# Kernel tuning notes

Hardware: AMD Instinct MI355X
Metric: run time of the kernel (lower is better)

The kernel has to match this reference:

```python
import jax, jax.numpy as jnp
import numpy as np

TOPK_R = 32  # topk_R from init


def setup_inputs() -> dict:
    key = jax.random.key(0)
    k1, k2 = jax.random.split(key)
    B, N, L_in, L_out = 8, 2048, 512, 512
    x = jax.random.normal(k1, (B, N, L_in), dtype=jnp.float32)
    # kaiming-uniform-style init for Linear weight [out, in]
    bound = float(np.sqrt(6.0 / L_in))
    W = jax.random.uniform(k2, (L_out, L_in), dtype=jnp.float32, minval=-bound, maxval=bound)
    return {"x": x, "W": W}


def reference(x, W):
    # x: [B, N, L_in]; W: [L_out, L_in] (Linear, no bias)
    xp = jnp.einsum('bnl,ol->bno', x, W)          # [B, N, L_out]
    # sim_score with norm=False: plain dot product
    score = jnp.einsum('bnd,bmd->bnm', xp, xp)    # [B, N, N]
    B, N, _ = score.shape
    # RkNNAdjacency: identity + top-k neighbors per row set to 1
    topk_idx = jax.lax.top_k(score, TOPK_R)[1]    # [B, N, k]
    adj = jnp.broadcast_to(jnp.eye(N, dtype=score.dtype), (B, N, N))
    b_idx = jnp.arange(B)[:, None, None]
    n_idx = jnp.arange(N)[None, :, None]
    adj = adj.at[b_idx, n_idx, topk_idx].set(1.0)
    # mask: 1 where neighbor, -1e19 elsewhere; NOTE: multiplicative mask (mask * score)
    mask = jnp.where(adj == 1.0, jnp.ones_like(adj), jnp.full_like(adj, -1e19))
    attention = jax.nn.softmax(mask * score, axis=2)  # [B, N, N]
    h = jnp.einsum('bnm,bmd->bnd', attention, xp)     # [B, N, L_out]
    return (h, attention)
```

## Files before the change

### kernel.cpp

```cpp
#include <hip/hip_runtime.h>
#include <cfloat>


typedef short bf16x8 __attribute__((ext_vector_type(8)));
typedef _Float16 f16x8 __attribute__((ext_vector_type(8)));
typedef _Float16 f16x4 __attribute__((ext_vector_type(4)));
typedef float f32x4 __attribute__((ext_vector_type(4)));

#define NX4 2097152
#define NW4 65536

__device__ __forceinline__ unsigned short f2bf(float f) {
  unsigned int u = __float_as_uint(f);
  unsigned int r = (u + 0x7FFFu + ((u >> 16) & 1u)) >> 16;
  return (unsigned short)r;
}

__device__ __forceinline__ void gload_lds16(const unsigned short* g, unsigned short* l) {
  __builtin_amdgcn_global_load_lds(
      (const __attribute__((address_space(1))) unsigned int*)g,
      (__attribute__((address_space(3))) unsigned int*)l, 16, 0, 0);
}

__device__ __forceinline__ unsigned int skey(float v, int m) {
  unsigned int u = __float_as_uint(v);
  u ^= ((unsigned int)((int)u >> 31)) | 0x80000000u;
  return (u & 0xFFFFF800u) | (unsigned int)m;
}

__global__ __launch_bounds__(256) void split_kernel(const float* __restrict__ x,
                                                    const float* __restrict__ W,
                                                    _Float16* __restrict__ xh,
                                                    _Float16* __restrict__ xl,
                                                    _Float16* __restrict__ wh,
                                                    _Float16* __restrict__ wl) {
  const int idx = blockIdx.x * 256 + threadIdx.x;
  if (idx >= NX4 + NW4) return;
  const bool isx = idx < NX4;
  const int i4 = isx ? idx : idx - NX4;
  const float4 v = isx ? reinterpret_cast<const float4*>(x)[i4]
                       : reinterpret_cast<const float4*>(W)[i4];
  f16x4 hv, lv;
  const float vv[4] = {v.x, v.y, v.z, v.w};
#pragma unroll
  for (int c = 0; c < 4; ++c) {
    const _Float16 h = (_Float16)vv[c];
    hv[c] = h;
    lv[c] = (_Float16)((vv[c] - (float)h) * 2048.0f);
  }
  if (isx) {
    reinterpret_cast<f16x4*>(xh)[i4] = hv;
    reinterpret_cast<f16x4*>(xl)[i4] = lv;
  } else {
    reinterpret_cast<f16x4*>(wh)[i4] = hv;
    reinterpret_cast<f16x4*>(wl)[i4] = lv;
  }
}

__global__ __launch_bounds__(256, 2) void gemm_xw_mfma(const unsigned short* __restrict__ xh,
                                                       const unsigned short* __restrict__ xl,
                                                       const unsigned short* __restrict__ wh,
                                                       const unsigned short* __restrict__ wl,
                                                       float* __restrict__ xp,
                                                       unsigned short* __restrict__ xp16) {
  __shared__ unsigned short lAh[2][128 * 32];
  __shared__ unsigned short lAl[2][128 * 32];
  __shared__ unsigned short lBh[2][128 * 32];
  __shared__ unsigned short lBl[2][128 * 32];
  const int tid = threadIdx.x;
  const int wid = tid >> 6, lane = tid & 63;
  const int lr = lane & 15, kg = lane >> 4;
  const int nbase = blockIdx.x * 128;
  const int obase = blockIdx.y * 128;
  const int wr = wid >> 1, wc = wid & 1;

  const int srow = tid >> 2;
  const int scol = (tid & 3) * 8;
  const unsigned short* gAh0 = xh + (size_t)(nbase + srow) * 512 + scol;
  const unsigned short* gAh1 = xh + (size_t)(nbase + 64 + srow) * 512 + scol;
  const unsigned short* gAl0 = xl + (size_t)(nbase + srow) * 512 + scol;
  const unsigned short* gAl1 = xl + (size_t)(nbase + 64 + srow) * 512 + scol;
  const unsigned short* gBh0 = wh + (size_t)(obase + srow) * 512 + scol;
  const unsigned short* gBh1 = wh + (size_t)(obase + 64 + srow) * 512 + scol;
  const unsigned short* gBl0 = wl + (size_t)(obase + srow) * 512 + scol;
  const unsigned short* gBl1 = wl + (size_t)(obase + 64 + srow) * 512 + scol;

  f32x4 acc_hh[4][4] = {};
  f32x4 acc_x[4][4] = {};

#define K1_STAGE(KB, BUF)                                  \
  do {                                                     \
    gload_lds16(gAh0 + (KB), &lAh[BUF][wid * 512]);        \
    gload_lds16(gAh1 + (KB), &lAh[BUF][2048 + wid * 512]); \
    gload_lds16(gAl0 + (KB), &lAl[BUF][wid * 512]);        \
    gload_lds16(gAl1 + (KB), &lAl[BUF][2048 + wid * 512]); \
    gload_lds16(gBh0 + (KB), &lBh[BUF][wid * 512]);        \
    gload_lds16(gBh1 + (KB), &lBh[BUF][2048 + wid * 512]); \
    gload_lds16(gBl0 + (KB), &lBl[BUF][wid * 512]);        \
    gload_lds16(gBl1 + (KB), &lBl[BUF][2048 + wid * 512]); \
  } while (0)

#define K1_COMPUTE(BUF)                                                                \
  do {                                                                                 \
    f16x8 ah[4], al[4], bh[4], bl[4];                                                  \
    _Pragma("unroll") for (int i2 = 0; i2 < 4; ++i2) {                                 \
      ah[i2] = *reinterpret_cast<const f16x8*>(&lAh[BUF][(wr * 64 + i2 * 16 + lr) * 32 + kg * 8]); \
      al[i2] = *reinterpret_cast<const f16x8*>(&lAl[BUF][(wr * 64 + i2 * 16 + lr) * 32 + kg * 8]); \
      bh[i2] = *reinterpret_cast<const f16x8*>(&lBh[BUF][(wc * 64 + i2 * 16 + lr) * 32 + kg * 8]); \
      bl[i2] = *reinterpret_cast<const f16x8*>(&lBl[BUF][(wc * 64 + i2 * 16 + lr) * 32 + kg * 8]); \
    }                                                                                  \
    _Pragma("unroll") for (int i2 = 0; i2 < 4; ++i2)                                   \
        _Pragma("unroll") for (int j2 = 0; j2 < 4; ++j2) {                             \
      acc_hh[i2][j2] = __builtin_amdgcn_mfma_f32_16x16x32_f16(ah[i2], bh[j2], acc_hh[i2][j2], 0, 0, 0); \
      acc_x[i2][j2] = __builtin_amdgcn_mfma_f32_16x16x32_f16(ah[i2], bl[j2], acc_x[i2][j2], 0, 0, 0);   \
      acc_x[i2][j2] = __builtin_amdgcn_mfma_f32_16x16x32_f16(al[i2], bh[j2], acc_x[i2][j2], 0, 0, 0);   \
    }                                                                                  \
  } while (0)

  K1_STAGE(0, 0);
  __syncthreads();
  for (int t = 0; t < 15; ++t) {
    K1_STAGE((t + 1) * 32, (t & 1) ^ 1);
    K1_COMPUTE(t & 1);
    __syncthreads();
  }
  K1_COMPUTE(1);

#pragma unroll
  for (int i = 0; i < 4; ++i) {
#pragma unroll
    for (int j = 0; j < 4; ++j) {
#pragma unroll
      for (int r = 0; r < 4; ++r) {
        const float v = acc_hh[i][j][r] + acc_x[i][j][r] * (1.0f / 2048.0f);
        const size_t row = (size_t)(nbase + wr * 64 + i * 16 + kg * 4 + r);
        const int col = obase + wc * 64 + j * 16 + lr;
        xp[row * 512 + col] = v;
        xp16[row * 512 + col] = f2bf(v);
      }
    }
  }
#undef K1_STAGE
#undef K1_COMPUTE
}

__global__ __launch_bounds__(256) void score_kernel(const unsigned short* __restrict__ xp16,
                                                    unsigned int* __restrict__ cand) {
  __shared__ unsigned short lA[2][128 * 32];
  __shared__ unsigned short lB[2][128 * 32];
  const int tid = threadIdx.x;
  const int wid = tid >> 6, lane = tid & 63;
  const int lr = lane & 15, kg = lane >> 4;
  const int b = blockIdx.x & 7;
  int p = blockIdx.x >> 3;
  int tn = 0, rem = 16;
  while (p >= rem) { p -= rem; rem--; tn++; }
  const int tm = tn + p;
  const int nbase = tn * 128, mbase = tm * 128;
  const unsigned short* Xb = xp16 + (size_t)b * 2048 * 512;
  const int wr = wid >> 1, wc = wid & 1;

  const int srow = tid >> 2;
  const int scol = (tid & 3) * 8;
  const unsigned short* gA0 = Xb + (size_t)(nbase + srow) * 512 + scol;
  const unsigned short* gA1 = Xb + (size_t)(nbase + 64 + srow) * 512 + scol;
  const unsigned short* gB0 = Xb + (size_t)(mbase + srow) * 512 + scol;
  const unsigned short* gB1 = Xb + (size_t)(mbase + 64 + srow) * 512 + scol;

  f32x4 acc[4][4] = {};

#define STAGE(KB, BUF)                                    \
  do {                                                    \
    gload_lds16(gA0 + (KB), &lA[BUF][wid * 512]);         \
    gload_lds16(gA1 + (KB), &lA[BUF][2048 + wid * 512]);  \
    gload_lds16(gB0 + (KB), &lB[BUF][wid * 512]);         \
    gload_lds16(gB1 + (KB), &lB[BUF][2048 + wid * 512]);  \
  } while (0)

#define COMPUTE(BUF)                                                                   \
  do {                                                                                 \
    bf16x8 af[4], bfr[4];                                                              \
    _Pragma("unroll") for (int i2 = 0; i2 < 4; ++i2) {                                 \
      af[i2] = *reinterpret_cast<const bf16x8*>(&lA[BUF][(wr * 64 + i2 * 16 + lr) * 32 + kg * 8]); \
      bfr[i2] = *reinterpret_cast<const bf16x8*>(&lB[BUF][(wc * 64 + i2 * 16 + lr) * 32 + kg * 8]); \
    }                                                                                  \
    _Pragma("unroll") for (int i2 = 0; i2 < 4; ++i2)                                   \
        _Pragma("unroll") for (int j2 = 0; j2 < 4; ++j2)                               \
            acc[i2][j2] =                                                              \
                __builtin_amdgcn_mfma_f32_16x16x32_bf16(af[i2], bfr[j2], acc[i2][j2], 0, 0, 0); \
  } while (0)

  STAGE(0, 0);
  __syncthreads();
  for (int t = 0; t < 15; ++t) {
    STAGE((t + 1) * 32, (t & 1) ^ 1);
    COMPUTE(t & 1);
    __syncthreads();
  }
  COMPUTE(1);

  const int mcol = mbase + wc * 64 + lr;
#pragma unroll
  for (int i = 0; i < 4; ++i) {
#pragma unroll
    for (int r = 0; r < 4; ++r) {
      const unsigned int x0 = skey(acc[i][0][r], mcol + 0);
      const unsigned int x1 = skey(acc[i][1][r], mcol + 16);
      const unsigned int x2 = skey(acc[i][2][r], mcol + 32);
      const unsigned int x3 = skey(acc[i][3][r], mcol + 48);
      const unsigned int lo01 = min(x0, x1), hi01 = max(x0, x1);
      const unsigned int lo23 = min(x2, x3), hi23 = max(x2, x3);
      unsigned int k1 = min(lo01, lo23);
      unsigned int k2 = min(max(lo01, lo23), min(hi01, hi23));
#pragma unroll
      for (int off = 1; off < 16; off <<= 1) {
        const unsigned int o1 = (unsigned int)__shfl_xor((int)k1, off);
        const unsigned int o2 = (unsigned int)__shfl_xor((int)k2, off);
        const unsigned int nk1 = min(k1, o1);
        const unsigned int nk2 = min(max(k1, o1), min(k2, o2));
        k1 = nk1;
        k2 = nk2;
      }
      if (lr == 0) {
        const int n = nbase + wr * 64 + i * 16 + kg * 4 + r;
        const uint2 kv = {k1, k2};
        *reinterpret_cast<uint2*>(cand + ((size_t)b * 2048 + n) * 512 + (tm * 2 + wc) * 2) = kv;
      }
    }
  }

  if (tn != tm) {
    const int nrow0 = nbase + wr * 64 + kg * 4;
#pragma unroll
    for (int j = 0; j < 4; ++j) {
      unsigned int k1 = 0xFFFFFFFFu, k2 = 0xFFFFFFFFu;
#pragma unroll
      for (int i = 0; i < 4; ++i) {
#pragma unroll
        for (int r = 0; r < 4; ++r) {
          const unsigned int xk = skey(acc[i][j][r], nrow0 + i * 16 + r);
          const unsigned int nk1 = min(k1, xk);
          k2 = min(k2, max(k1, xk));
          k1 = nk1;
        }
      }
#pragma unroll
      for (int off = 16; off < 64; off <<= 1) {
        const unsigned int o1 = (unsigned int)__shfl_xor((int)k1, off);
        const unsigned int o2 = (unsigned int)__shfl_xor((int)k2, off);
        const unsigned int nk1 = min(k1, o1);
        const unsigned int nk2 = min(max(k1, o1), min(k2, o2));
        k1 = nk1;
        k2 = nk2;
      }
      if (kg == 0) {
        const int m = mbase + wc * 64 + j * 16 + lr;
        const uint2 kv = {k1, k2};
        *reinterpret_cast<uint2*>(cand + ((size_t)b * 2048 + m) * 512 + (tn * 2 + wr) * 2) = kv;
      }
    }
  }
#undef STAGE
#undef COMPUTE
}

__global__ __launch_bounds__(64) void finalize_kernel(const float* __restrict__ xp,
                                                      float* __restrict__ h,
                                                      float* __restrict__ att) {
  const int l = threadIdx.x;
  const int b = blockIdx.x & 7;
  const int n = blockIdx.x >> 3;
  const size_t r = (size_t)b * 2048 + n;

  unsigned int key = reinterpret_cast<const unsigned int*>(h + r * 512)[l];
  int wsel[8];
#pragma unroll
  for (int t = 0; t < 8; ++t) {
    unsigned int m = key;
#pragma unroll
    for (int off = 1; off < 64; off <<= 1)
      m = min(m, (unsigned int)__shfl_xor((int)m, off));
    wsel[t] = (int)(m & 0x7FFu);
    if (key == m) key = 0xFFFFFFFFu;
  }

  const float* xb = xp + (size_t)b * 2048 * 512;
  const float* xn = xb + (size_t)n * 512;
  const float4 q0 = reinterpret_cast<const float4*>(xn)[2 * l];
  const float4 q1 = reinterpret_cast<const float4*>(xn)[2 * l + 1];

  float bestv = FLT_MAX;
  int besti = 0x7fffffff;
#pragma unroll
  for (int t = 0; t < 8; ++t) {
    const float* xm = xb + (size_t)wsel[t] * 512;
    const float4 p0 = reinterpret_cast<const float4*>(xm)[2 * l];
    const float4 p1 = reinterpret_cast<const float4*>(xm)[2 * l + 1];
    float s = 0.f;
    s = fmaf(q0.x, p0.x, s); s = fmaf(q0.y, p0.y, s);
    s = fmaf(q0.z, p0.z, s); s = fmaf(q0.w, p0.w, s);
    s = fmaf(q1.x, p1.x, s); s = fmaf(q1.y, p1.y, s);
    s = fmaf(q1.z, p1.z, s); s = fmaf(q1.w, p1.w, s);
#pragma unroll
    for (int off = 1; off < 64; off <<= 1) s += __shfl_xor(s, off);
    if (s < bestv || (s == bestv && wsel[t] < besti)) { bestv = s; besti = wsel[t]; }
  }

  const float* xs = xb + (size_t)besti * 512;
  const float4 w0 = reinterpret_cast<const float4*>(xs)[2 * l];
  const float4 w1 = reinterpret_cast<const float4*>(xs)[2 * l + 1];
  float* hrow = h + r * 512;
  reinterpret_cast<float4*>(hrow)[2 * l] = w0;
  reinterpret_cast<float4*>(hrow)[2 * l + 1] = w1;

  float* arow = att + r * 2048;
#pragma unroll
  for (int s = 0; s < 8; ++s) {
    const int cbase = s * 256 + l * 4;
    float4 v;
    v.x = (cbase + 0 == besti) ? 1.0f : 0.0f;
    v.y = (cbase + 1 == besti) ? 1.0f : 0.0f;
    v.z = (cbase + 2 == besti) ? 1.0f : 0.0f;
    v.w = (cbase + 3 == besti) ? 1.0f : 0.0f;
    reinterpret_cast<float4*>(arow)[s * 64 + l] = v;
  }
}

extern "C" void kernel_launch(void* const* d_in, const int* in_sizes, int n_in,
                              void* d_out, int out_size, void* d_ws, size_t ws_size,
                              hipStream_t stream) {
  const float* x = (const float*)d_in[0];
  const float* W = (const float*)d_in[1];
  float* out = (float*)d_out;
  float* h = out;
  float* att = out + (size_t)8 * 2048 * 512;
  float* xp = (float*)d_ws;

  char* attb = (char*)att;
  _Float16* xh = (_Float16*)(attb + 0);
  _Float16* xl = (_Float16*)(attb + (size_t)16 * 1024 * 1024);
  _Float16* wh = (_Float16*)(attb + (size_t)32 * 1024 * 1024);
  _Float16* wl = (_Float16*)(attb + (size_t)33 * 1024 * 1024);
  unsigned short* xp16 = (unsigned short*)(attb + (size_t)112 * 1024 * 1024);

  hipLaunchKernelGGL(split_kernel, dim3((NX4 + NW4 + 255) / 256), dim3(256), 0, stream,
                     x, W, xh, xl, wh, wl);

  hipLaunchKernelGGL(gemm_xw_mfma, dim3(16384 / 128, 512 / 128), dim3(256), 0, stream,
                     (const unsigned short*)xh, (const unsigned short*)xl,
                     (const unsigned short*)wh, (const unsigned short*)wl, xp, xp16);

  hipLaunchKernelGGL(score_kernel, dim3(8 * 136), dim3(256), 0, stream, xp16,
                     (unsigned int*)h);

  hipLaunchKernelGGL(finalize_kernel, dim3(16384), dim3(64), 0, stream, xp, h, att);
}
```

Baseline: 124.6 us.

## Fuse x fp16 hi/lo split into the projection GEMM's A-tile load

The separate pass that splits all of x into fp16 high/low halves is removed. The GEMM now loads fp32 x tiles into registers, splits them in-kernel and writes them to LDS, overlapped with the MFMA compute on the other buffer. Only W is still pre-split. This avoids a 32MB read and 32MB write round trip through global memory. In exchange the GEMM reads fp32 A four times, once per output column block, and does extra conversion ALU work and register-staged LDS stores in its loop.

```diff
diff --git a/kernel.cpp b/kernel.cpp
--- a/kernel.cpp
+++ b/kernel.cpp
@@ -7,7 +7,6 @@
 typedef _Float16 f16x4 __attribute__((ext_vector_type(4)));
 typedef float f32x4 __attribute__((ext_vector_type(4)));
 
-#define NX4 2097152
 #define NW4 65536
 
 __device__ __forceinline__ unsigned short f2bf(float f) {
@@ -28,18 +27,12 @@
   return (u & 0xFFFFF800u) | (unsigned int)m;
 }
 
-__global__ __launch_bounds__(256) void split_kernel(const float* __restrict__ x,
-                                                    const float* __restrict__ W,
-                                                    _Float16* __restrict__ xh,
-                                                    _Float16* __restrict__ xl,
-                                                    _Float16* __restrict__ wh,
-                                                    _Float16* __restrict__ wl) {
-  const int idx = blockIdx.x * 256 + threadIdx.x;
-  if (idx >= NX4 + NW4) return;
-  const bool isx = idx < NX4;
-  const int i4 = isx ? idx : idx - NX4;
-  const float4 v = isx ? reinterpret_cast<const float4*>(x)[i4]
-                       : reinterpret_cast<const float4*>(W)[i4];
+__global__ __launch_bounds__(256) void splitW_kernel(const float* __restrict__ W,
+                                                     _Float16* __restrict__ wh,
+                                                     _Float16* __restrict__ wl) {
+  const int i4 = blockIdx.x * 256 + threadIdx.x;
+  if (i4 >= NW4) return;
+  const float4 v = reinterpret_cast<const float4*>(W)[i4];
   f16x4 hv, lv;
   const float vv[4] = {v.x, v.y, v.z, v.w};
 #pragma unroll
@@ -48,17 +41,11 @@
     hv[c] = h;
     lv[c] = (_Float16)((vv[c] - (float)h) * 2048.0f);
   }
-  if (isx) {
-    reinterpret_cast<f16x4*>(xh)[i4] = hv;
-    reinterpret_cast<f16x4*>(xl)[i4] = lv;
-  } else {
-    reinterpret_cast<f16x4*>(wh)[i4] = hv;
-    reinterpret_cast<f16x4*>(wl)[i4] = lv;
-  }
-}
-
-__global__ __launch_bounds__(256, 2) void gemm_xw_mfma(const unsigned short* __restrict__ xh,
-                                                       const unsigned short* __restrict__ xl,
+  reinterpret_cast<f16x4*>(wh)[i4] = hv;
+  reinterpret_cast<f16x4*>(wl)[i4] = lv;
+}
+
+__global__ __launch_bounds__(256, 2) void gemm_xw_mfma(const float* __restrict__ x,
                                                        const unsigned short* __restrict__ wh,
                                                        const unsigned short* __restrict__ wl,
                                                        float* __restrict__ xp,
@@ -76,10 +63,8 @@
 
   const int srow = tid >> 2;
   const int scol = (tid & 3) * 8;
-  const unsigned short* gAh0 = xh + (size_t)(nbase + srow) * 512 + scol;
-  const unsigned short* gAh1 = xh + (size_t)(nbase + 64 + srow) * 512 + scol;
-  const unsigned short* gAl0 = xl + (size_t)(nbase + srow) * 512 + scol;
-  const unsigned short* gAl1 = xl + (size_t)(nbase + 64 + srow) * 512 + scol;
+  const float* gX0 = x + (size_t)(nbase + srow) * 512 + scol;
+  const float* gX1 = x + (size_t)(nbase + 64 + srow) * 512 + scol;
   const unsigned short* gBh0 = wh + (size_t)(obase + srow) * 512 + scol;
   const unsigned short* gBh1 = wh + (size_t)(obase + 64 + srow) * 512 + scol;
   const unsigned short* gBl0 = wl + (size_t)(obase + srow) * 512 + scol;
@@ -87,13 +72,37 @@
 
   f32x4 acc_hh[4][4] = {};
   f32x4 acc_x[4][4] = {};
-
-#define K1_STAGE(KB, BUF)                                  \
+  float4 va[4];
+
+#define K1_LOADA(KB)                                                \
+  do {                                                              \
+    va[0] = *reinterpret_cast<const float4*>(gX0 + (KB));           \
+    va[1] = *reinterpret_cast<const float4*>(gX0 + (KB) + 4);       \
+    va[2] = *reinterpret_cast<const float4*>(gX1 + (KB));           \
+    va[3] = *reinterpret_cast<const float4*>(gX1 + (KB) + 4);       \
+  } while (0)
+
+#define K1_WRITEA(BUF)                                              \
+  do {                                                              \
+    _Pragma("unroll") for (int p = 0; p < 2; ++p) {                 \
+      f16x8 hv, lv;                                                 \
+      _Pragma("unroll") for (int q = 0; q < 2; ++q) {               \
+        const float vv[4] = {va[2 * p + q].x, va[2 * p + q].y,      \
+                             va[2 * p + q].z, va[2 * p + q].w};     \
+        _Pragma("unroll") for (int c = 0; c < 4; ++c) {             \
+          const _Float16 hh = (_Float16)vv[c];                      \
+          hv[4 * q + c] = hh;                                       \
+          lv[4 * q + c] = (_Float16)((vv[c] - (float)hh) * 2048.0f);\
+        }                                                           \
+      }                                                             \
+      const int ra = (srow + 64 * p) * 32 + scol;                   \
+      *reinterpret_cast<f16x8*>(&lAh[BUF][ra]) = hv;                \
+      *reinterpret_cast<f16x8*>(&lAl[BUF][ra]) = lv;                \
+    }                                                               \
+  } while (0)
+
+#define K1_STAGEB(KB, BUF)                                 \
   do {                                                     \
-    gload_lds16(gAh0 + (KB), &lAh[BUF][wid * 512]);        \
-    gload_lds16(gAh1 + (KB), &lAh[BUF][2048 + wid * 512]); \
-    gload_lds16(gAl0 + (KB), &lAl[BUF][wid * 512]);        \
-    gload_lds16(gAl1 + (KB), &lAl[BUF][2048 + wid * 512]); \
     gload_lds16(gBh0 + (KB), &lBh[BUF][wid * 512]);        \
     gload_lds16(gBh1 + (KB), &lBh[BUF][2048 + wid * 512]); \
     gload_lds16(gBl0 + (KB), &lBl[BUF][wid * 512]);        \
@@ -117,11 +126,15 @@
     }                                                                                  \
   } while (0)
 
-  K1_STAGE(0, 0);
+  K1_LOADA(0);
+  K1_STAGEB(0, 0);
+  K1_WRITEA(0);
   __syncthreads();
   for (int t = 0; t < 15; ++t) {
-    K1_STAGE((t + 1) * 32, (t & 1) ^ 1);
+    K1_LOADA((t + 1) * 32);
+    K1_STAGEB((t + 1) * 32, (t & 1) ^ 1);
     K1_COMPUTE(t & 1);
+    K1_WRITEA((t & 1) ^ 1);
     __syncthreads();
   }
   K1_COMPUTE(1);
@@ -140,7 +153,9 @@
       }
     }
   }
-#undef K1_STAGE
+#undef K1_LOADA
+#undef K1_WRITEA
+#undef K1_STAGEB
 #undef K1_COMPUTE
 }
 
@@ -337,18 +352,14 @@
   float* xp = (float*)d_ws;
 
   char* attb = (char*)att;
-  _Float16* xh = (_Float16*)(attb + 0);
-  _Float16* xl = (_Float16*)(attb + (size_t)16 * 1024 * 1024);
   _Float16* wh = (_Float16*)(attb + (size_t)32 * 1024 * 1024);
   _Float16* wl = (_Float16*)(attb + (size_t)33 * 1024 * 1024);
   unsigned short* xp16 = (unsigned short*)(attb + (size_t)112 * 1024 * 1024);
 
-  hipLaunchKernelGGL(split_kernel, dim3((NX4 + NW4 + 255) / 256), dim3(256), 0, stream,
-                     x, W, xh, xl, wh, wl);
+  hipLaunchKernelGGL(splitW_kernel, dim3(NW4 / 256), dim3(256), 0, stream, W, wh, wl);
 
   hipLaunchKernelGGL(gemm_xw_mfma, dim3(16384 / 128, 512 / 128), dim3(256), 0, stream,
-                     (const unsigned short*)xh, (const unsigned short*)xl,
-                     (const unsigned short*)wh, (const unsigned short*)wl, xp, xp16);
+                     x, (const unsigned short*)wh, (const unsigned short*)wl, xp, xp16);
 
   hipLaunchKernelGGL(score_kernel, dim3(8 * 136), dim3(256), 0, stream, xp16,
                      (unsigned int*)h);
```

Result: faster. 117.9 us, median of 2 (-5.4%).
